# Optimization experiments

Hardware: AMD Instinct MI355X
Metric: run time of the kernel (lower is better)

The kernel has to match this reference:

```python
import jax, jax.numpy as jnp
import numpy as np

N = 50000      # nodes
E_R = 800000   # random edges (plus N self-loops appended)
F = 128        # input feature dim
HD = 256       # base hidden dim
D = 64         # gnn_dim (per-head out channels)
H = 4          # attention heads
A = 32         # n_actions
LEAKY = 0.2    # PyG GATv2 negative_slope default
LN_EPS = 1e-5


def _ln(x, g, b):
    mu = x.mean(-1, keepdims=True)
    v = ((x - mu) ** 2).mean(-1, keepdims=True)
    return (x - mu) / jnp.sqrt(v + LN_EPS) * g + b


def _gatv2(x, src, dst, wl, wr, att, wres, bias):
    # GATv2Conv, concat=False (mean over heads), residual=True, no edge_attr.
    xl = (x @ wl).reshape(-1, H, D)   # [N,H,D] source transform
    xr = (x @ wr).reshape(-1, H, D)   # [N,H,D] target transform
    m = jax.nn.leaky_relu(xl[src] + xr[dst], LEAKY)          # [E,H,D]
    e = jnp.einsum('ehd,hd->eh', m, att)                     # [E,H]
    emax = jax.ops.segment_max(e, dst, num_segments=N)       # [N,H]
    p = jnp.exp(e - emax[dst])
    denom = jax.ops.segment_sum(p, dst, num_segments=N)      # [N,H]
    alpha = p / denom[dst]                                   # segment softmax
    out = jax.ops.segment_sum(alpha[..., None] * xl[src], dst, num_segments=N)
    out = out.mean(axis=1)                                   # concat=False -> head mean
    return out + x @ wres + bias                             # residual + bias


def setup_inputs() -> dict:
    key = jax.random.key(0)
    ks = jax.random.split(key, 16)
    inputs = jax.random.normal(ks[0], (N, F), jnp.float32)
    src_r = jax.random.randint(ks[1], (E_R,), 0, N, jnp.int32)
    dst_r = jax.random.randint(ks[2], (E_R,), 0, N, jnp.int32)
    loops = jnp.arange(N, dtype=jnp.int32)  # add_self_loops=True default in PyG
    src = jnp.concatenate([src_r, loops])
    dst = jnp.concatenate([dst_r, loops])
    w = lambda k, s: jax.random.normal(k, s, jnp.float32) * 0.05
    return {
        'inputs': inputs, 'src': src, 'dst': dst,
        'w0': w(ks[3], (F, HD)), 'b0': jnp.zeros((HD,)), 'g0': jnp.ones((HD,)), 'be0': jnp.zeros((HD,)),
        'w1': w(ks[4], (HD, HD)), 'b1': jnp.zeros((HD,)), 'g1': jnp.ones((HD,)), 'be1': jnp.zeros((HD,)),
        'wl1': w(ks[5], (HD, H * D)), 'wr1': w(ks[6], (HD, H * D)), 'att1': w(ks[7], (H, D)),
        'wres1': w(ks[8], (HD, D)), 'bias1': jnp.zeros((D,)), 'lg1': jnp.ones((D,)), 'lb1': jnp.zeros((D,)),
        'wl2': w(ks[9], (D, H * D)), 'wr2': w(ks[10], (D, H * D)), 'att2': w(ks[11], (H, D)),
        'wres2': w(ks[12], (D, D)), 'bias2': jnp.zeros((D,)), 'lg2': jnp.ones((D,)), 'lb2': jnp.zeros((D,)),
        'wa': w(ks[13], (D, A)), 'ba': jnp.zeros((A,)),
    }


def reference(inputs, src, dst, w0, b0, g0, be0, w1, b1, g1, be1,
              wl1, wr1, att1, wres1, bias1, lg1, lb1,
              wl2, wr2, att2, wres2, bias2, lg2, lb2, wa, ba):
    # base MLP: (Linear + ReLU + LayerNorm) x 2
    x = _ln(jax.nn.relu(inputs @ w0 + b0), g0, be0)
    x = _ln(jax.nn.relu(x @ w1 + b1), g1, be1)
    # GATv2 stack: (GATv2Conv + ReLU + LayerNorm) x 2
    h = _ln(jax.nn.relu(_gatv2(x, src, dst, wl1, wr1, att1, wres1, bias1)), lg1, lb1)
    h = _ln(jax.nn.relu(_gatv2(h, src, dst, wl2, wr2, att2, wres2, bias2)), lg2, lb2)
    q = h @ wa + ba
    return q
```

## Files before the change

kernel.cpp:

```cpp
#include <hip/hip_runtime.h>
#include <stdint.h>

#define LEAKY 0.2f
#define LN_EPS 1e-5f
#define BF16_ONES 0x3F803F80u

extern "C" __global__ void GNNAgentV2_84834194031328_kernel() {}

typedef __attribute__((ext_vector_type(8))) short short8;
typedef __attribute__((ext_vector_type(4))) float f32x4;
typedef _Float16 f16x2 __attribute__((ext_vector_type(2)));

__device__ __forceinline__ float bfbits2f(uint32_t bits){
    union { uint32_t u; float f; } c; c.u = bits; return c.f;
}
__device__ __forceinline__ float bf2f(uint16_t u){ return bfbits2f(((uint32_t)u) << 16); }
__device__ __forceinline__ uint16_t f2bf(float f){
    union { float f; uint32_t u; } c; c.f = f;
    uint32_t u = c.u;
    return (uint16_t)((u + 0x7fffu + ((u >> 16) & 1u)) >> 16);
}
__device__ __forceinline__ uint16_t f2h(float f){
    _Float16 h = (_Float16)f;
    return __builtin_bit_cast(uint16_t, h);
}
__device__ __forceinline__ f16x2 u2h2(uint32_t u){ return __builtin_bit_cast(f16x2, u); }
__device__ __forceinline__ void ld_bf16x4(const uint16_t* p, float* o){
    uint2 v = *(const uint2*)p;
    o[0] = bfbits2f(v.x << 16);
    o[1] = bfbits2f(v.x & 0xffff0000u);
    o[2] = bfbits2f(v.y << 16);
    o[3] = bfbits2f(v.y & 0xffff0000u);
}
__device__ __forceinline__ void st_bf16x4(uint16_t* p, float a, float b, float c, float d){
    uint2 v;
    v.x = (uint32_t)f2bf(a) | ((uint32_t)f2bf(b) << 16);
    v.y = (uint32_t)f2bf(c) | ((uint32_t)f2bf(d) << 16);
    *(uint2*)p = v;
}

__device__ __forceinline__ float dot2acc(f16x2 a, f16x2 b, float c){
#if __has_builtin(__builtin_amdgcn_fdot2)
    return __builtin_amdgcn_fdot2(a, b, c, false);
#else
    c = fmaf((float)a.x, (float)b.x, c);
    return fmaf((float)a.y, (float)b.y, c);
#endif
}

template<int CTRL>
__device__ __forceinline__ float dpp_add(float v){
    int x = __builtin_amdgcn_update_dpp(0, __builtin_bit_cast(int, v), CTRL, 0xF, 0xF, true);
    return v + __builtin_bit_cast(float, x);
}
template<int CTRL>
__device__ __forceinline__ float dpp_mov(float v){
    int x = __builtin_amdgcn_update_dpp(0, __builtin_bit_cast(int, v), CTRL, 0xF, 0xF, true);
    return __builtin_bit_cast(float, x);
}

struct Seg { const void* src; uint16_t* dst; int K; int N; int colOff; };
struct SegTable { Seg s[22]; };

__global__ void k_front(SegTable st, const uint32_t* __restrict__ g0w,
                        const int* __restrict__ dst, int* __restrict__ counts, int E, int nbE)
{
    int b = blockIdx.x;
    if (b < nbE){
        int e = b * 256 + threadIdx.x;
        if (e < E) atomicAdd(&counts[dst[e]], 1);
        return;
    }
    b -= nbE;
    {
        int isbf = (*g0w == BF16_ONES) ? 1 : 0;
        Seg sg = st.s[b >> 8];
        int elems = sg.K * sg.N;
        int idx = (b & 255) * 256 + threadIdx.x;
        if (idx >= elems) return;
        float v = isbf ? bf2f(((const uint16_t*)sg.src)[idx]) : ((const float*)sg.src)[idx];
        if (sg.K == 1){
            sg.dst[idx] = f2bf(v);
            return;
        }
        int k = idx / sg.N, c = idx - k * sg.N;
        int cg = sg.colOff + c;
        int ct = cg >> 6, c64 = cg & 63;
        int cf = c64 >> 4, l15 = c64 & 15;
        int kf = k >> 5, r = k & 31;
        int quad = r >> 3, j = r & 7;
        size_t off = (size_t)ct * sg.K * 64 + kf * 2048 + cf * 512 + (quad * 16 + l15) * 8 + j;
        sg.dst[off] = f2bf(v);
    }
}

__global__ void k_scan1(const int* __restrict__ counts, int* __restrict__ offs,
                        int* __restrict__ bsums, int n){
    __shared__ int sd[256];
    int t = threadIdx.x;
    int base = blockIdx.x * 1024 + t * 4;
    int v0 = (base + 0 < n) ? counts[base + 0] : 0;
    int v1 = (base + 1 < n) ? counts[base + 1] : 0;
    int v2 = (base + 2 < n) ? counts[base + 2] : 0;
    int v3 = (base + 3 < n) ? counts[base + 3] : 0;
    int tsum = v0 + v1 + v2 + v3;
    sd[t] = tsum;
    __syncthreads();
    for (int off = 1; off < 256; off <<= 1){
        int x = 0;
        if (t >= off) x = sd[t - off];
        __syncthreads();
        sd[t] += x;
        __syncthreads();
    }
    int run = sd[t] - tsum;
    if (base + 0 < n){ offs[base + 0] = run; } run += v0;
    if (base + 1 < n){ offs[base + 1] = run; } run += v1;
    if (base + 2 < n){ offs[base + 2] = run; } run += v2;
    if (base + 3 < n){ offs[base + 3] = run; }
    if (t == 255) bsums[blockIdx.x] = sd[255];
}
__global__ void k_scan23(const int* __restrict__ bsums, int* __restrict__ offs,
                         int* __restrict__ cursor, int n){
    int lane = threadIdx.x & 63;
    int idx = blockIdx.x >> 2;
    int total = 0;
    for (int base = 0; base < idx; base += 64){
        int v = (base + lane < idx) ? bsums[base + lane] : 0;
        v += __shfl_xor(v, 1);  v += __shfl_xor(v, 2);  v += __shfl_xor(v, 4);
        v += __shfl_xor(v, 8);  v += __shfl_xor(v, 16); v += __shfl_xor(v, 32);
        total += v;
    }
    int i = blockIdx.x * 256 + threadIdx.x;
    if (i < n){
        int o = offs[i] + total;
        offs[i] = o;
        cursor[i] = o;
    }
}
__global__ void k_scatter(const int* __restrict__ src, const int* __restrict__ dst,
                          int* __restrict__ cursor, int* __restrict__ csr_src, int E){
    int e = blockIdx.x * 256 + threadIdx.x;
    if (e < E){
        int p = atomicAdd(&cursor[dst[e]], 1);
        csr_src[p] = src[e];
    }
}

template<int K, int CG, bool BIAS_RELU, bool OUT_F16, bool AF32>
__global__ __launch_bounds__(256, 4) void k_gemm(
    const uint16_t* __restrict__ A,
    const uint16_t* __restrict__ Bp,
    const uint16_t* __restrict__ bias,
    uint16_t* __restrict__ o0, int ld0,
    uint16_t* __restrict__ o1, int ld1,
    uint16_t* __restrict__ o2, int ld2,
    int s1, int s2,
    int n,
    const uint32_t* __restrict__ g0w, int want)
{
    if (want >= 0){
        int isbf = (*g0w == BF16_ONES) ? 1 : 0;
        if (isbf != want) return;
    }
    constexpr int PITCH = K + 8;
    __shared__ __align__(16) uint16_t SMEM[64 * PITCH];
    uint16_t* As = SMEM;
    uint16_t* Cs = SMEM;
    int t = threadIdx.x;
    int row0 = blockIdx.x * 64;
    int ctBase = blockIdx.y * CG;

    constexpr int KC = K / 8;
    if (AF32){
        const float* Af = (const float*)A;
        for (int c = t; c < 64 * KC; c += 256){
            int r = c / KC, kc = c - r * KC;
            int gr = row0 + r;
            uint4 v = make_uint4(0, 0, 0, 0);
            if (gr < n){
                const float* p = Af + (size_t)gr * K + kc * 8;
                float4 fa = *(const float4*)p;
                float4 fb = *(const float4*)(p + 4);
                v.x = (uint32_t)f2bf(fa.x) | ((uint32_t)f2bf(fa.y) << 16);
                v.y = (uint32_t)f2bf(fa.z) | ((uint32_t)f2bf(fa.w) << 16);
                v.z = (uint32_t)f2bf(fb.x) | ((uint32_t)f2bf(fb.y) << 16);
                v.w = (uint32_t)f2bf(fb.z) | ((uint32_t)f2bf(fb.w) << 16);
            }
            *(uint4*)(As + r * PITCH + kc * 8) = v;
        }
    } else {
        for (int c = t; c < 64 * KC; c += 256){
            int r = c / KC, kc = c - r * KC;
            uint4 v = make_uint4(0, 0, 0, 0);
            int gr = row0 + r;
            if (gr < n) v = *(const uint4*)(A + (size_t)gr * K + kc * 8);
            *(uint4*)(As + r * PITCH + kc * 8) = v;
        }
    }

    int lane = t & 63, wv = t >> 6;
    int quad = lane >> 4, l15 = lane & 15;
    int wrow = wv * 16;

    __syncthreads();

    constexpr int KF = K / 32;
    short8 areg[KF];
    #pragma unroll
    for (int kf = 0; kf < KF; ++kf)
        areg[kf] = __builtin_bit_cast(short8,
            *(const uint4*)(As + (wrow + l15) * PITCH + kf * 32 + quad * 8));

    __syncthreads();

    for (int g = 0; g < CG; ++g){
        int ct = ctBase + g;
        const uint16_t* Bb = Bp + (size_t)ct * K * 64 + (size_t)lane * 8;

        f32x4 acc[4];
        #pragma unroll
        for (int j = 0; j < 4; ++j) acc[j] = (f32x4){0.f, 0.f, 0.f, 0.f};

        short8 bcur[4], bnxt[4];
        #pragma unroll
        for (int cf = 0; cf < 4; ++cf)
            bcur[cf] = __builtin_bit_cast(short8, *(const uint4*)(Bb + cf * 512));

        #pragma unroll
        for (int kf = 0; kf < KF; ++kf){
            if (kf + 1 < KF){
                #pragma unroll
                for (int cf = 0; cf < 4; ++cf)
                    bnxt[cf] = __builtin_bit_cast(short8,
                        *(const uint4*)(Bb + (kf + 1) * 2048 + cf * 512));
            }
            #pragma unroll
            for (int cf = 0; cf < 4; ++cf)
                acc[cf] = __builtin_amdgcn_mfma_f32_16x16x32_bf16(areg[kf], bcur[cf], acc[cf], 0, 0, 0);
            if (kf + 1 < KF){
                #pragma unroll
                for (int cf = 0; cf < 4; ++cf) bcur[cf] = bnxt[cf];
            }
        }

        #pragma unroll
        for (int r = 0; r < 4; ++r){
            #pragma unroll
            for (int cf = 0; cf < 4; ++cf){
                float v = acc[cf][r];
                if (BIAS_RELU){
                    v += bf2f(bias[ct * 64 + cf * 16 + l15]);
                    v = v > 0.f ? v : 0.f;
                }
                Cs[(wrow + quad * 4 + r) * 72 + cf * 16 + l15] = OUT_F16 ? f2h(v) : f2bf(v);
            }
        }

        uint16_t* obase; int ld, colOut;
        if (ct < s1)      { obase = o0; ld = ld0; colOut = ct * 64; }
        else if (ct < s2) { obase = o1; ld = ld1; colOut = (ct - s1) * 64; }
        else              { obase = o2; ld = ld2; colOut = (ct - s2) * 64; }

        #pragma unroll
        for (int it = 0; it < 2; ++it){
            int i = it * 64 + lane;
            int row = wrow + (i >> 3);
            int sg = i & 7;
            int grow = row0 + row;
            if (grow < n){
                uint4 v = *(const uint4*)(Cs + row * 72 + sg * 8);
                *(uint4*)(obase + (size_t)grow * ld + colOut + sg * 8) = v;
            }
        }
    }
}

__global__ __launch_bounds__(256) void k_ln256(
    uint16_t* __restrict__ x, const uint16_t* __restrict__ g,
    const uint16_t* __restrict__ be, int n)
{
    int t = threadIdx.x;
    int lane = t & 63, wv = t >> 6;
    int row = blockIdx.x * 8 + wv * 2;
    int c0 = lane * 4;
    float gv[4], bev[4];
    ld_bf16x4(g + c0, gv);
    ld_bf16x4(be + c0, bev);
    #pragma unroll
    for (int rr = 0; rr < 2; ++rr){
        int r = row + rr;
        if (r >= n) continue;
        float v[4];
        ld_bf16x4(x + (size_t)r * 256 + c0, v);
        float s1 = v[0] + v[1] + v[2] + v[3];
        float s2 = v[0]*v[0] + v[1]*v[1] + v[2]*v[2] + v[3]*v[3];
        #pragma unroll
        for (int m = 1; m < 64; m <<= 1){
            s1 += __shfl_xor(s1, m);
            s2 += __shfl_xor(s2, m);
        }
        float mean = s1 * (1.f / 256.f);
        float var  = s2 * (1.f / 256.f) - mean * mean;
        float rstd = rsqrtf(var + LN_EPS);
        st_bf16x4(x + (size_t)r * 256 + c0,
                  (v[0] - mean) * rstd * gv[0] + bev[0],
                  (v[1] - mean) * rstd * gv[1] + bev[1],
                  (v[2] - mean) * rstd * gv[2] + bev[2],
                  (v[3] - mean) * rstd * gv[3] + bev[3]);
    }
}

__global__ __launch_bounds__(128) void k_gat_aggregate(
    const uint16_t* __restrict__ xl, const uint16_t* __restrict__ xr,
    const uint16_t* __restrict__ res,
    const uint16_t* __restrict__ att,
    const uint16_t* __restrict__ bias,
    const uint16_t* __restrict__ lg, const uint16_t* __restrict__ lb,
    const int* __restrict__ offs, const int* __restrict__ counts, const int* __restrict__ csr_src,
    uint16_t* __restrict__ out, int n)
{
    int node = __builtin_amdgcn_readfirstlane((blockIdx.x << 1) + (threadIdx.x >> 6));
    if (node >= n) return;
    int lane = threadIdx.x & 63;
    int c0 = lane * 4;
    uint2 xrv = *(const uint2*)(xr + (size_t)node * 256 + c0);
    f16x2 xr0 = u2h2(xrv.x), xr1 = u2h2(xrv.y);
    float av[4];
    ld_bf16x4(att + c0, av);
    f16x2 av0 = { (_Float16)av[0], (_Float16)av[1] };
    f16x2 av1 = { (_Float16)av[2], (_Float16)av[3] };
    const f16x2 lk2 = { (_Float16)LEAKY, (_Float16)LEAKY };
    bool par1 = (lane & 1) != 0, par2 = (lane & 2) != 0;
    int start = offs[node], cnt = counts[node];
    float lsum = 0.f;
    float a0 = 0.f, a1 = 0.f, a2 = 0.f, a3 = 0.f;

    #define EDGE_SCORE_H(xa, xb, e)                                      \
    {                                                                    \
        f16x2 u0 = xa + xr0, u1 = xb + xr1;                              \
        f16x2 m0 = __builtin_elementwise_max(u0, u0 * lk2);              \
        f16x2 m1 = __builtin_elementwise_max(u1, u1 * lk2);              \
        e = dot2acc(m0, av0, dot2acc(m1, av1, 0.f));                     \
    }
    #define FOLD4(e0, e1, e2, e3, z)                                     \
    {                                                                    \
        float b01 = par1 ? e0 : e1;                                      \
        float z01 = (par1 ? e1 : e0) + dpp_mov<0xB1>(b01);               \
        float b23 = par1 ? e2 : e3;                                      \
        float z23 = (par1 ? e3 : e2) + dpp_mov<0xB1>(b23);               \
        float bz = par2 ? z01 : z23;                                     \
        z  = (par2 ? z23 : z01) + dpp_mov<0x4E>(bz);                     \
        z += dpp_mov<0x124>(z);                           \
        z += dpp_mov<0x128>(z);                           \
    }

    int j = 0;
    if (cnt >= 8){
        int i0 = csr_src[start + 0];
        int i1 = csr_src[start + 1];
        int i2 = csr_src[start + 2];
        int i3 = csr_src[start + 3];
        int i4 = csr_src[start + 4];
        int i5 = csr_src[start + 5];
        int i6 = csr_src[start + 6];
        int i7 = csr_src[start + 7];
        while (true){
            int t0 = __builtin_amdgcn_readfirstlane(i0);
            int t1 = __builtin_amdgcn_readfirstlane(i1);
            int t2 = __builtin_amdgcn_readfirstlane(i2);
            int t3 = __builtin_amdgcn_readfirstlane(i3);
            int t4 = __builtin_amdgcn_readfirstlane(i4);
            int t5 = __builtin_amdgcn_readfirstlane(i5);
            int t6 = __builtin_amdgcn_readfirstlane(i6);
            int t7 = __builtin_amdgcn_readfirstlane(i7);
            int jn = j + 8;
            bool more = (jn + 7 < cnt);
            if (more){
                i0 = csr_src[start + jn + 0];
                i1 = csr_src[start + jn + 1];
                i2 = csr_src[start + jn + 2];
                i3 = csr_src[start + jn + 3];
                i4 = csr_src[start + jn + 4];
                i5 = csr_src[start + jn + 5];
                i6 = csr_src[start + jn + 6];
                i7 = csr_src[start + jn + 7];
            }
            f16x2 x0a, x0b, x1a, x1b, x2a, x2b, x3a, x3b;
            f16x2 x4a, x4b, x5a, x5b, x6a, x6b, x7a, x7b;
            { uint2 v = *(const uint2*)(xl + (size_t)(uint32_t)t0 * 256 + c0); x0a = u2h2(v.x); x0b = u2h2(v.y); }
            { uint2 v = *(const uint2*)(xl + (size_t)(uint32_t)t1 * 256 + c0); x1a = u2h2(v.x); x1b = u2h2(v.y); }
            { uint2 v = *(const uint2*)(xl + (size_t)(uint32_t)t2 * 256 + c0); x2a = u2h2(v.x); x2b = u2h2(v.y); }
            { uint2 v = *(const uint2*)(xl + (size_t)(uint32_t)t3 * 256 + c0); x3a = u2h2(v.x); x3b = u2h2(v.y); }
            { uint2 v = *(const uint2*)(xl + (size_t)(uint32_t)t4 * 256 + c0); x4a = u2h2(v.x); x4b = u2h2(v.y); }
            { uint2 v = *(const uint2*)(xl + (size_t)(uint32_t)t5 * 256 + c0); x5a = u2h2(v.x); x5b = u2h2(v.y); }
            { uint2 v = *(const uint2*)(xl + (size_t)(uint32_t)t6 * 256 + c0); x6a = u2h2(v.x); x6b = u2h2(v.y); }
            { uint2 v = *(const uint2*)(xl + (size_t)(uint32_t)t7 * 256 + c0); x7a = u2h2(v.x); x7b = u2h2(v.y); }
            float e0, e1, e2, e3, e4, e5, e6, e7;
            EDGE_SCORE_H(x0a, x0b, e0); EDGE_SCORE_H(x1a, x1b, e1);
            EDGE_SCORE_H(x2a, x2b, e2); EDGE_SCORE_H(x3a, x3b, e3);
            EDGE_SCORE_H(x4a, x4b, e4); EDGE_SCORE_H(x5a, x5b, e5);
            EDGE_SCORE_H(x6a, x6b, e6); EDGE_SCORE_H(x7a, x7b, e7);
            float zA, zB;
            FOLD4(e0, e1, e2, e3, zA);
            FOLD4(e4, e5, e6, e7, zB);
            float pzA = __expf(zA);
            float pzB = __expf(zB);
            float p0 = dpp_mov<0x00>(pzA);
            float p1 = dpp_mov<0x55>(pzA);
            float p2 = dpp_mov<0xAA>(pzA);
            float p3 = dpp_mov<0xFF>(pzA);
            float p4 = dpp_mov<0x00>(pzB);
            float p5 = dpp_mov<0x55>(pzB);
            float p6 = dpp_mov<0xAA>(pzB);
            float p7 = dpp_mov<0xFF>(pzB);
            a0 = fmaf((float)x0a.x, p0, a0); a0 = fmaf((float)x1a.x, p1, a0);
            a0 = fmaf((float)x2a.x, p2, a0); a0 = fmaf((float)x3a.x, p3, a0);
            a0 = fmaf((float)x4a.x, p4, a0); a0 = fmaf((float)x5a.x, p5, a0);
            a0 = fmaf((float)x6a.x, p6, a0); a0 = fmaf((float)x7a.x, p7, a0);
            a1 = fmaf((float)x0a.y, p0, a1); a1 = fmaf((float)x1a.y, p1, a1);
            a1 = fmaf((float)x2a.y, p2, a1); a1 = fmaf((float)x3a.y, p3, a1);
            a1 = fmaf((float)x4a.y, p4, a1); a1 = fmaf((float)x5a.y, p5, a1);
            a1 = fmaf((float)x6a.y, p6, a1); a1 = fmaf((float)x7a.y, p7, a1);
            a2 = fmaf((float)x0b.x, p0, a2); a2 = fmaf((float)x1b.x, p1, a2);
            a2 = fmaf((float)x2b.x, p2, a2); a2 = fmaf((float)x3b.x, p3, a2);
            a2 = fmaf((float)x4b.x, p4, a2); a2 = fmaf((float)x5b.x, p5, a2);
            a2 = fmaf((float)x6b.x, p6, a2); a2 = fmaf((float)x7b.x, p7, a2);
            a3 = fmaf((float)x0b.y, p0, a3); a3 = fmaf((float)x1b.y, p1, a3);
            a3 = fmaf((float)x2b.y, p2, a3); a3 = fmaf((float)x3b.y, p3, a3);
            a3 = fmaf((float)x4b.y, p4, a3); a3 = fmaf((float)x5b.y, p5, a3);
            a3 = fmaf((float)x6b.y, p6, a3); a3 = fmaf((float)x7b.y, p7, a3);
            lsum += ((p0 + p1) + (p2 + p3)) + ((p4 + p5) + (p6 + p7));
            j = jn;
            if (!more) break;
        }
    }
    if (cnt - j >= 4){
        int i0 = csr_src[start + j + 0];
        int i1 = csr_src[start + j + 1];
        int i2 = csr_src[start + j + 2];
        int i3 = csr_src[start + j + 3];
        int t0 = __builtin_amdgcn_readfirstlane(i0);
        int t1 = __builtin_amdgcn_readfirstlane(i1);
        int t2 = __builtin_amdgcn_readfirstlane(i2);
        int t3 = __builtin_amdgcn_readfirstlane(i3);
        f16x2 x0a, x0b, x1a, x1b, x2a, x2b, x3a, x3b;
        { uint2 v = *(const uint2*)(xl + (size_t)(uint32_t)t0 * 256 + c0); x0a = u2h2(v.x); x0b = u2h2(v.y); }
        { uint2 v = *(const uint2*)(xl + (size_t)(uint32_t)t1 * 256 + c0); x1a = u2h2(v.x); x1b = u2h2(v.y); }
        { uint2 v = *(const uint2*)(xl + (size_t)(uint32_t)t2 * 256 + c0); x2a = u2h2(v.x); x2b = u2h2(v.y); }
        { uint2 v = *(const uint2*)(xl + (size_t)(uint32_t)t3 * 256 + c0); x3a = u2h2(v.x); x3b = u2h2(v.y); }
        float e0, e1, e2, e3;
        EDGE_SCORE_H(x0a, x0b, e0); EDGE_SCORE_H(x1a, x1b, e1);
        EDGE_SCORE_H(x2a, x2b, e2); EDGE_SCORE_H(x3a, x3b, e3);
        float z;
        FOLD4(e0, e1, e2, e3, z);
        float pz = __expf(z);
        float p0 = dpp_mov<0x00>(pz);
        float p1 = dpp_mov<0x55>(pz);
        float p2 = dpp_mov<0xAA>(pz);
        float p3 = dpp_mov<0xFF>(pz);
        a0 = fmaf((float)x0a.x, p0, a0); a0 = fmaf((float)x1a.x, p1, a0);
        a0 = fmaf((float)x2a.x, p2, a0); a0 = fmaf((float)x3a.x, p3, a0);
        a1 = fmaf((float)x0a.y, p0, a1); a1 = fmaf((float)x1a.y, p1, a1);
        a1 = fmaf((float)x2a.y, p2, a1); a1 = fmaf((float)x3a.y, p3, a1);
        a2 = fmaf((float)x0b.x, p0, a2); a2 = fmaf((float)x1b.x, p1, a2);
        a2 = fmaf((float)x2b.x, p2, a2); a2 = fmaf((float)x3b.x, p3, a2);
        a3 = fmaf((float)x0b.y, p0, a3); a3 = fmaf((float)x1b.y, p1, a3);
        a3 = fmaf((float)x2b.y, p2, a3); a3 = fmaf((float)x3b.y, p3, a3);
        lsum += (p0 + p1) + (p2 + p3);
        j += 4;
    }
    for (; j < cnt; ++j){
        int t0 = __builtin_amdgcn_readfirstlane(csr_src[start + j]);
        uint2 v = *(const uint2*)(xl + (size_t)(uint32_t)t0 * 256 + c0);
        f16x2 xa = u2h2(v.x), xb = u2h2(v.y);
        float e0;
        EDGE_SCORE_H(xa, xb, e0);
        e0 = dpp_add<0xB1>(e0);
        e0 = dpp_add<0x4E>(e0);
        e0 = dpp_add<0x141>(e0);
        e0 = dpp_add<0x140>(e0);
        float p0 = __expf(e0);
        a0 = fmaf((float)xa.x, p0, a0);
        a1 = fmaf((float)xa.y, p0, a1);
        a2 = fmaf((float)xb.x, p0, a2);
        a3 = fmaf((float)xb.y, p0, a3);
        lsum += p0;
    }
    #undef EDGE_SCORE_H
    #undef FOLD4

    float inv = 1.f / lsum;
    a0 *= inv; a1 *= inv; a2 *= inv; a3 *= inv;
    a0 += __shfl_xor(a0, 16); a0 += __shfl_xor(a0, 32);
    a1 += __shfl_xor(a1, 16); a1 += __shfl_xor(a1, 32);
    a2 += __shfl_xor(a2, 16); a2 += __shfl_xor(a2, 32);
    a3 += __shfl_xor(a3, 16); a3 += __shfl_xor(a3, 32);
    a0 *= 0.25f; a1 *= 0.25f; a2 *= 0.25f; a3 *= 0.25f;
    int d0 = (lane & 15) * 4;
    uint2 rv = *(const uint2*)(res + (size_t)node * 64 + d0);
    f16x2 r01 = u2h2(rv.x), r23 = u2h2(rv.y);
    float bvv[4];
    ld_bf16x4(bias + d0, bvv);
    float v0 = a0 + (float)r01.x + bvv[0]; v0 = v0 > 0.f ? v0 : 0.f;
    float v1 = a1 + (float)r01.y + bvv[1]; v1 = v1 > 0.f ? v1 : 0.f;
    float v2 = a2 + (float)r23.x + bvv[2]; v2 = v2 > 0.f ? v2 : 0.f;
    float v3 = a3 + (float)r23.y + bvv[3]; v3 = v3 > 0.f ? v3 : 0.f;
    float s1 = v0 + v1 + v2 + v3;
    float s2 = v0*v0 + v1*v1 + v2*v2 + v3*v3;
    s1 += __shfl_xor(s1, 1); s2 += __shfl_xor(s2, 1);
    s1 += __shfl_xor(s1, 2); s2 += __shfl_xor(s2, 2);
    s1 += __shfl_xor(s1, 4); s2 += __shfl_xor(s2, 4);
    s1 += __shfl_xor(s1, 8); s2 += __shfl_xor(s2, 8);
    float mean = s1 * (1.f / 64.f);
    float var  = s2 * (1.f / 64.f) - mean * mean;
    float rstd = rsqrtf(var + LN_EPS);
    if (lane < 16){
        float gvv[4], bev[4];
        ld_bf16x4(lg + d0, gvv);
        ld_bf16x4(lb + d0, bev);
        st_bf16x4(out + (size_t)node * 64 + d0,
                  (v0 - mean) * rstd * gvv[0] + bev[0],
                  (v1 - mean) * rstd * gvv[1] + bev[1],
                  (v2 - mean) * rstd * gvv[2] + bev[2],
                  (v3 - mean) * rstd * gvv[3] + bev[3]);
    }
}

__global__ __launch_bounds__(256) void k_final(
    const uint16_t* __restrict__ h, const void* __restrict__ wa,
    const void* __restrict__ ba, void* __restrict__ out, int n,
    const uint32_t* __restrict__ g0w)
{
    __shared__ float was[64][32];
    __shared__ float bas[32];
    __shared__ float hs[8][64];
    int t = threadIdx.x;
    int isbf = (*g0w == BF16_ONES) ? 1 : 0;
    for (int i = t; i < 64 * 32; i += 256)
        was[i >> 5][i & 31] = isbf ? bf2f(((const uint16_t*)wa)[i]) : ((const float*)wa)[i];
    if (t < 32) bas[t] = isbf ? bf2f(((const uint16_t*)ba)[t]) : ((const float*)ba)[t];
    int row0 = blockIdx.x * 8;
    for (int i = t; i < 8 * 64; i += 256){
        int r = i >> 6, k = i & 63;
        int rr = row0 + r;
        hs[r][k] = (rr < n) ? bf2f(h[(size_t)rr * 64 + k]) : 0.f;
    }
    __syncthreads();
    int r = t >> 5, c = t & 31;
    float acc = bas[c];
    #pragma unroll
    for (int k = 0; k < 64; ++k) acc += hs[r][k] * was[k][c];
    int node = row0 + r;
    if (node < n){
        if (isbf) ((uint16_t*)out)[(size_t)node * 32 + c] = f2bf(acc);
        else      ((float*)out)[(size_t)node * 32 + c] = acc;
    }
}

extern "C" void kernel_launch(void* const* d_in, const int* in_sizes, int n_in,
                              void* d_out, int out_size, void* d_ws, size_t ws_size,
                              hipStream_t stream)
{
    const int* src = (const int*)d_in[1];
    const int* dst = (const int*)d_in[2];
    const uint32_t* g0w = (const uint32_t*)d_in[5];
    const int N = in_sizes[0] / 128;
    const int E = in_sizes[1];

    char* base = (char*)d_ws;
    size_t off = 0;
    auto alloc = [&](size_t bytes) -> void* {
        void* p = base + off;
        off += (bytes + 255) & ~(size_t)255;
        return p;
    };
    uint16_t* X0   = (uint16_t*)alloc((size_t)N * 256 * 2);
    uint16_t* X1   = (uint16_t*)alloc((size_t)N * 256 * 2);
    uint16_t* XL   = (uint16_t*)alloc((size_t)N * 256 * 2);
    uint16_t* XR   = (uint16_t*)alloc((size_t)N * 256 * 2);
    uint16_t* RES  = (uint16_t*)alloc((size_t)N * 64 * 2);
    uint16_t* w0P  = (uint16_t*)alloc(256 * 128 * 2);
    uint16_t* w1P  = (uint16_t*)alloc(256 * 256 * 2);
    uint16_t* wt1P = (uint16_t*)alloc(576 * 256 * 2);
    uint16_t* wt2P = (uint16_t*)alloc(576 * 64 * 2);
    uint16_t* VEC  = (uint16_t*)alloc(4096 * 2);
    int* counts    = (int*)alloc((size_t)N * 4);
    int* offs      = (int*)alloc((size_t)N * 4);
    int* cursor    = (int*)alloc((size_t)N * 4);
    int* bsums     = (int*)alloc(4096);
    int* csr_src   = (int*)alloc((size_t)E * 4);

    uint16_t* H1 = X0;
    uint16_t* H2 = X0 + (size_t)N * 64;

    const int vB0=0, vG0=256, vBE0=512, vB1=768, vG1=1024, vBE1=1280;
    const int vATT1=1536, vBIAS1=1792, vLG1=1856, vLB1=1920;
    const int vATT2=1984, vBIAS2=2240, vLG2=2304, vLB2=2368;

    SegTable st;
    int si = 0;
    auto seg = [&](int i, uint16_t* d, int K, int Nn, int colOff){
        st.s[si++] = { d_in[i], d, K, Nn, colOff };
    };
    seg(3,  w0P, 128, 256, 0);
    seg(7,  w1P, 256, 256, 0);
    seg(11, wt1P, 256, 256, 0);
    seg(12, wt1P, 256, 256, 256);
    seg(14, wt1P, 256, 64, 512);
    seg(18, wt2P, 64, 256, 0);
    seg(19, wt2P, 64, 256, 256);
    seg(21, wt2P, 64, 64, 512);
    seg(4,  VEC+vB0, 1, 256, 0);  seg(5,  VEC+vG0, 1, 256, 0);  seg(6,  VEC+vBE0, 1, 256, 0);
    seg(8,  VEC+vB1, 1, 256, 0);  seg(9,  VEC+vG1, 1, 256, 0);  seg(10, VEC+vBE1, 1, 256, 0);
    seg(13, VEC+vATT1, 1, 256, 0); seg(15, VEC+vBIAS1, 1, 64, 0);
    seg(16, VEC+vLG1, 1, 64, 0);   seg(17, VEC+vLB1, 1, 64, 0);
    seg(20, VEC+vATT2, 1, 256, 0); seg(22, VEC+vBIAS2, 1, 64, 0);
    seg(23, VEC+vLG2, 1, 64, 0);   seg(24, VEC+vLB2, 1, 64, 0);

    const int nbE = (E + 255) / 256;
    const int nb_scan  = (N + 1023) / 1024;
    const int nb_nodes = (N + 255) / 256;

    hipMemsetAsync(counts, 0, (size_t)N * 4, stream);
    k_front<<<nbE + 22 * 256, 256, 0, stream>>>(st, g0w, dst, counts, E, nbE);

    k_scan1<<<nb_scan, 256, 0, stream>>>(counts, offs, bsums, N);
    k_scan23<<<nb_nodes, 256, 0, stream>>>(bsums, offs, cursor, N);
    k_scatter<<<nbE, 256, 0, stream>>>(src, dst, cursor, csr_src, E);

    const int rt = (N + 63) / 64;
    const int nb_ln  = (N + 7) / 8;
    const int nb_agg = (N + 1) / 2;

    k_gemm<128, 4, true, false, false><<<rt, 256, 0, stream>>>(
        (const uint16_t*)d_in[0], w0P, VEC+vB0, X0,256, X0,256, X0,256, 99, 99, N, g0w, 1);
    k_gemm<128, 4, true, false, true><<<rt, 256, 0, stream>>>(
        (const uint16_t*)d_in[0], w0P, VEC+vB0, X0,256, X0,256, X0,256, 99, 99, N, g0w, 0);
    k_ln256<<<nb_ln, 256, 0, stream>>>(X0, VEC+vG0, VEC+vBE0, N);
    k_gemm<256, 4, true, false, false><<<rt, 256, 0, stream>>>(
        X0, w1P, VEC+vB1, X1,256, X1,256, X1,256, 99, 99, N, nullptr, -1);
    k_ln256<<<nb_ln, 256, 0, stream>>>(X1, VEC+vG1, VEC+vBE1, N);

    k_gemm<256, 9, false, true, false><<<rt, 256, 0, stream>>>(
        X1, wt1P, nullptr, XL,256, XR,256, RES,64, 4, 8, N, nullptr, -1);
    k_gat_aggregate<<<nb_agg, 128, 0, stream>>>(XL, XR, RES,
        VEC+vATT1, VEC+vBIAS1, VEC+vLG1, VEC+vLB1, offs, counts, csr_src, H1, N);

    k_gemm<64, 9, false, true, false><<<rt, 256, 0, stream>>>(
        H1, wt2P, nullptr, XL,256, XR,256, RES,64, 4, 8, N, nullptr, -1);
    k_gat_aggregate<<<nb_agg, 128, 0, stream>>>(XL, XR, RES,
        VEC+vATT2, VEC+vBIAS2, VEC+vLG2, VEC+vLB2, offs, counts, csr_src, H2, N);

    k_final<<<nb_ln, 256, 0, stream>>>(H2, d_in[25], d_in[26], d_out, N, g0w);
}
```

Before: 477.4 us.

## Double GEMM row tile to 128 rows so each wave computes two row fragments

The GEMM kernel now handles 128 rows per block instead of 64. Each wave holds two 16-row A fragments and reuses every loaded B fragment for two MFMAs, which halves global B-weight traffic per output row. The cost is more registers and LDS per block (launch bounds lowered to 2 blocks per SIMD) and half as many blocks, so occupancy and latency hiding may suffer.

```diff
diff --git a/kernel.cpp b/kernel.cpp
--- a/kernel.cpp
+++ b/kernel.cpp
@@ -148,7 +148,7 @@
 }
 
 template<int K, int CG, bool BIAS_RELU, bool OUT_F16, bool AF32>
-__global__ __launch_bounds__(256, 4) void k_gemm(
+__global__ __launch_bounds__(256, 2) void k_gemm(
     const uint16_t* __restrict__ A,
     const uint16_t* __restrict__ Bp,
     const uint16_t* __restrict__ bias,
@@ -164,17 +164,20 @@
         if (isbf != want) return;
     }
     constexpr int PITCH = K + 8;
-    __shared__ __align__(16) uint16_t SMEM[64 * PITCH];
+    constexpr int SA = 128 * PITCH;
+    constexpr int SC = 128 * 72;
+    constexpr int SELEMS = (SA > SC) ? SA : SC;
+    __shared__ __align__(16) uint16_t SMEM[SELEMS];
     uint16_t* As = SMEM;
     uint16_t* Cs = SMEM;
     int t = threadIdx.x;
-    int row0 = blockIdx.x * 64;
+    int row0 = blockIdx.x * 128;
     int ctBase = blockIdx.y * CG;
 
     constexpr int KC = K / 8;
     if (AF32){
         const float* Af = (const float*)A;
-        for (int c = t; c < 64 * KC; c += 256){
+        for (int c = t; c < 128 * KC; c += 256){
             int r = c / KC, kc = c - r * KC;
             int gr = row0 + r;
             uint4 v = make_uint4(0, 0, 0, 0);
@@ -190,7 +193,7 @@
             *(uint4*)(As + r * PITCH + kc * 8) = v;
         }
     } else {
-        for (int c = t; c < 64 * KC; c += 256){
+        for (int c = t; c < 128 * KC; c += 256){
             int r = c / KC, kc = c - r * KC;
             uint4 v = make_uint4(0, 0, 0, 0);
             int gr = row0 + r;
@@ -201,16 +204,18 @@
 
     int lane = t & 63, wv = t >> 6;
     int quad = lane >> 4, l15 = lane & 15;
-    int wrow = wv * 16;
+    int wrow = wv * 32;
 
     __syncthreads();
 
     constexpr int KF = K / 32;
-    short8 areg[KF];
+    short8 areg[2][KF];
     #pragma unroll
-    for (int kf = 0; kf < KF; ++kf)
-        areg[kf] = __builtin_bit_cast(short8,
-            *(const uint4*)(As + (wrow + l15) * PITCH + kf * 32 + quad * 8));
+    for (int rf = 0; rf < 2; ++rf)
+        #pragma unroll
+        for (int kf = 0; kf < KF; ++kf)
+            areg[rf][kf] = __builtin_bit_cast(short8,
+                *(const uint4*)(As + (wrow + rf * 16 + l15) * PITCH + kf * 32 + quad * 8));
 
     __syncthreads();
 
@@ -218,9 +223,11 @@
         int ct = ctBase + g;
         const uint16_t* Bb = Bp + (size_t)ct * K * 64 + (size_t)lane * 8;
 
-        f32x4 acc[4];
+        f32x4 acc[2][4];
         #pragma unroll
-        for (int j = 0; j < 4; ++j) acc[j] = (f32x4){0.f, 0.f, 0.f, 0.f};
+        for (int rf = 0; rf < 2; ++rf)
+            #pragma unroll
+            for (int j = 0; j < 4; ++j) acc[rf][j] = (f32x4){0.f, 0.f, 0.f, 0.f};
 
         short8 bcur[4], bnxt[4];
         #pragma unroll
@@ -236,8 +243,10 @@
                         *(const uint4*)(Bb + (kf + 1) * 2048 + cf * 512));
             }
             #pragma unroll
-            for (int cf = 0; cf < 4; ++cf)
-                acc[cf] = __builtin_amdgcn_mfma_f32_16x16x32_bf16(areg[kf], bcur[cf], acc[cf], 0, 0, 0);
+            for (int cf = 0; cf < 4; ++cf){
+                acc[0][cf] = __builtin_amdgcn_mfma_f32_16x16x32_bf16(areg[0][kf], bcur[cf], acc[0][cf], 0, 0, 0);
+                acc[1][cf] = __builtin_amdgcn_mfma_f32_16x16x32_bf16(areg[1][kf], bcur[cf], acc[1][cf], 0, 0, 0);
+            }
             if (kf + 1 < KF){
                 #pragma unroll
                 for (int cf = 0; cf < 4; ++cf) bcur[cf] = bnxt[cf];
@@ -245,15 +254,18 @@
         }
 
         #pragma unroll
-        for (int r = 0; r < 4; ++r){
+        for (int rf = 0; rf < 2; ++rf){
             #pragma unroll
-            for (int cf = 0; cf < 4; ++cf){
-                float v = acc[cf][r];
-                if (BIAS_RELU){
-                    v += bf2f(bias[ct * 64 + cf * 16 + l15]);
-                    v = v > 0.f ? v : 0.f;
+            for (int r = 0; r < 4; ++r){
+                #pragma unroll
+                for (int cf = 0; cf < 4; ++cf){
+                    float v = acc[rf][cf][r];
+                    if (BIAS_RELU){
+                        v += bf2f(bias[ct * 64 + cf * 16 + l15]);
+                        v = v > 0.f ? v : 0.f;
+                    }
+                    Cs[(wrow + rf * 16 + quad * 4 + r) * 72 + cf * 16 + l15] = OUT_F16 ? f2h(v) : f2bf(v);
                 }
-                Cs[(wrow + quad * 4 + r) * 72 + cf * 16 + l15] = OUT_F16 ? f2h(v) : f2bf(v);
             }
         }
 
@@ -263,7 +275,7 @@
         else              { obase = o2; ld = ld2; colOut = (ct - s2) * 64; }
 
         #pragma unroll
-        for (int it = 0; it < 2; ++it){
+        for (int it = 0; it < 4; ++it){
             int i = it * 64 + lane;
             int row = wrow + (i >> 3);
             int sg = i & 7;
@@ -629,7 +641,7 @@
     k_scan23<<<nb_nodes, 256, 0, stream>>>(bsums, offs, cursor, N);
     k_scatter<<<nbE, 256, 0, stream>>>(src, dst, cursor, csr_src, E);
 
-    const int rt = (N + 63) / 64;
+    const int rt = (N + 127) / 128;
     const int nb_ln  = (N + 7) / 8;
     const int nb_agg = (N + 1) / 2;
 
```

After: 463.4 us. 1.03x faster.
